# Optimization experiments

Hardware: AMD Instinct MI355X
Metric: run time of the kernel (lower is better)

The kernel has to match this reference:

```python
import jax, jax.numpy as jnp
import numpy as np

B, N, J, P = 64, 2048, 32, 64   # instances, ops per instance, jobs, ops per job (N = J*P)
D, H = 128, 128                 # out_size_ope, hidden_size_ope
NEG_SLOPE = 0.2


def _kaiming(key, fan_in, fan_out):
    return jax.random.normal(key, (fan_in, fan_out), jnp.float32) * np.sqrt(2.0 / fan_in)


def _mlp(x, W1, b1, W2, b2):
    # nn.Sequential(Linear, ELU, Linear)
    return jax.nn.elu(x @ W1 + b1) @ W2 + b2


def setup_inputs() -> dict:
    key = jax.random.key(0)
    ks = jax.random.split(key, 4)
    features = jax.random.normal(ks[0], (B, N, D), jnp.float32)
    job_starts = jnp.arange(J, dtype=jnp.int32) * P                      # first op of each job block
    offsets = jax.random.randint(ks[1], (B, J), 0, P)                    # current position within block
    ope_step_batch = job_starts[None, :] + offsets                       # [B, J], step_j in [start_j, end_j]
    end_ope_biases_batch = jnp.broadcast_to(job_starts + (P - 1), (B, J))
    opes_appertain_batch = jnp.broadcast_to(jnp.repeat(jnp.arange(J, dtype=jnp.int32), P)[None, :], (B, N))
    batch_idxes = jnp.arange(B, dtype=jnp.int32)
    inp = {
        'features': features,
        'discount_r': jnp.float32(0.9),
        'ope_step_batch': ope_step_batch,
        'end_ope_biases_batch': end_ope_biases_batch,
        'opes_appertain_batch': opes_appertain_batch,
        'batch_idxes': batch_idxes,
    }
    for i, nm in enumerate(['fw', 'zj', 'pr']):
        k1, k2 = jax.random.split(jax.random.fold_in(ks[2], i))
        inp[nm + '_W1'] = _kaiming(k1, D, H)
        inp[nm + '_b1'] = jnp.zeros((H,), jnp.float32)
        inp[nm + '_W2'] = _kaiming(k2, H, D)
        inp[nm + '_b2'] = jnp.zeros((D,), jnp.float32)
    return inp


def reference(features, discount_r,
              fw_W1, fw_b1, fw_W2, fw_b2,
              zj_W1, zj_b1, zj_W2, zj_b2,
              pr_W1, pr_b1, pr_W2, pr_b2,
              ope_step_batch, end_ope_biases_batch, opes_appertain_batch, batch_idxes):
    # opes_appertain_batch is accepted but unused, exactly like the torch forward.
    f32 = features.dtype
    steps = ope_step_batch[batch_idxes]        # [B, J]
    ends = end_ope_biases_batch[batch_idxes]   # [B, J]
    i = jnp.arange(N)

    # --- per-job descending update loop, vectorized ---
    # op i is updated iff step_j < i <= end_j for its job j; descending order in the
    # original means feat[i-1] is still the ORIGINAL value, so updates are independent.
    memb = (i[None, None, :] > steps[:, :, None]) & (i[None, None, :] <= ends[:, :, None])  # [B,J,N]
    updated = jnp.any(memb, axis=1)                                                         # [B,N]
    step_of = jnp.sum(jnp.where(memb, steps[:, :, None], 0), axis=1)                        # [B,N]
    rpow = discount_r ** (i[None, :] - step_of).astype(f32)                                 # r^(i - step)
    feat_prev = jnp.concatenate([jnp.zeros_like(features[:, :1]), features[:, :-1]], axis=1)
    # aggregate(MEAN): agg_f_w(feat_pre) + agg_f_w(feat_sub * r)
    cand = _mlp(features, fw_W1, fw_b1, fw_W2, fw_b2) + \
           _mlp(feat_prev * rpow[..., None], fw_W1, fw_b1, fw_W2, fw_b2)
    feat1 = jnp.where(updated[..., None], cand, features)

    # --- collect feat at each valid job's current step (step positions are never updated) ---
    collected = jax.vmap(lambda f, s: f[s])(features, steps)   # [B, J, D]
    valid = steps <= ends                                      # [B, J]
    n = jnp.sum(valid, axis=1).astype(f32)                     # [B]
    S = jnp.sum(jnp.where(valid[..., None], collected, 0.0), axis=1)  # [B, D]
    # aggregate_dif: new[j] = agg_z_j((old[j] + r * sum_{k!=j} old[k]) / n)
    mixed = (collected + discount_r * (S[:, None, :] - collected)) / n[:, None, None]
    z = _mlp(mixed, zj_W1, zj_b1, zj_W2, zj_b2)                # [B, J, D]

    # faithful replication of feat_opt[b][save_index[k]] = features_all[k]
    # (writes at op positions equal to JOB indices 0..J-1, for valid jobs)
    head = jnp.where(valid[..., None], z, feat1[:, :J, :])
    feat2 = feat1.at[:, :J, :].set(head)

    out = jax.nn.leaky_relu(_mlp(feat2, pr_W1, pr_b1, pr_W2, pr_b2), NEG_SLOPE)
    return out
```

## Files before the change

### kernel.cpp

```cpp
#include <hip/hip_runtime.h>

#define B_ 64
#define N_ 2048
#define J_ 32
#define D_ 128
#define NEG_SLOPE_ 0.2f

typedef __attribute__((ext_vector_type(4))) float f32x4;
typedef __attribute__((ext_vector_type(8))) __bf16 bf16x8;
typedef __attribute__((ext_vector_type(4))) __bf16 bf16x4;

#define ACT_NONE 0
#define ACT_ELU 1
#define ACT_LEAKY 2

template<int ACT>
__device__ __forceinline__ float apply_act(float v) {
    if constexpr (ACT == ACT_ELU)        return v > 0.f ? v : __expf(v) - 1.f;
    else if constexpr (ACT == ACT_LEAKY) return v >= 0.f ? v : NEG_SLOPE_ * v;
    else return v;
}

__device__ __forceinline__ bf16x8 frag_ld(const __bf16* src, int row, int kc) {
    return *(const bf16x8*)&src[row * D_ + ((kc ^ (row & 7)) << 3)];
}

__device__ __forceinline__ void load_wregs2(const __bf16* __restrict__ wmat,
                                            int wst, int ln, int lq, bf16x8 wr_[4][2]) {
#pragma unroll
    for (int ks = 0; ks < 4; ++ks)
#pragma unroll
        for (int mt = 0; mt < 2; ++mt)
            wr_[ks][mt] = frag_ld(wmat, wst * 32 + mt * 16 + ln, ks * 4 + lq);
}

__device__ __forceinline__ void st_row(__bf16* dst, int row, int ch,
                                       float4 f0, float4 f1, float s) {
    bf16x8 u;
    u[0] = (__bf16)(f0.x * s); u[1] = (__bf16)(f0.y * s);
    u[2] = (__bf16)(f0.z * s); u[3] = (__bf16)(f0.w * s);
    u[4] = (__bf16)(f1.x * s); u[5] = (__bf16)(f1.y * s);
    u[6] = (__bf16)(f1.z * s); u[7] = (__bf16)(f1.w * s);
    *(bf16x8*)&dst[row * D_ + ((ch ^ (row & 7)) << 3)] = u;
}

template<bool INIT>
__device__ __forceinline__ void gemmS32(const __bf16* xb, const bf16x8 wr_[4][2],
                                        int ln, int lq, f32x4 acc[2][2]) {
    if constexpr (INIT) {
        const f32x4 z = {0.f, 0.f, 0.f, 0.f};
        acc[0][0] = z; acc[0][1] = z; acc[1][0] = z; acc[1][1] = z;
    }
#pragma unroll
    for (int ks = 0; ks < 4; ++ks) {
        const int kc = ks * 4 + lq;
        const bf16x8 b0 = frag_ld(xb, ln, kc);
        const bf16x8 b1 = frag_ld(xb, 16 + ln, kc);
#pragma unroll
        for (int mt = 0; mt < 2; ++mt) {
            acc[mt][0] = __builtin_amdgcn_mfma_f32_16x16x32_bf16(wr_[ks][mt], b0, acc[mt][0], 0, 0, 0);
            acc[mt][1] = __builtin_amdgcn_mfma_f32_16x16x32_bf16(wr_[ks][mt], b1, acc[mt][1], 0, 0, 0);
        }
    }
}

template<int ACT>
__device__ __forceinline__ void epiS32_lds(const f32x4 acc[2][2], __bf16* dst, int rowoff,
                                           const float* __restrict__ bias,
                                           int wst, int ln, int lq) {
#pragma unroll
    for (int mt = 0; mt < 2; ++mt) {
        const int cb = wst * 32 + mt * 16 + lq * 4;
        const f32x4 bv = *(const f32x4*)&bias[cb];
#pragma unroll
        for (int nt = 0; nt < 2; ++nt) {
            const int jr = rowoff + nt * 16 + ln;
            bf16x4 o;
#pragma unroll
            for (int r = 0; r < 4; ++r)
                o[r] = (__bf16)apply_act<ACT>(acc[mt][nt][r] + bv[r]);
            *(bf16x4*)&dst[jr * D_ + (((cb >> 3) ^ (jr & 7)) << 3) + (cb & 7)] = o;
        }
    }
}

__global__ __launch_bounds__(256) void k_prep(
    const float* __restrict__ w0, const float* __restrict__ w1,
    const float* __restrict__ w2, const float* __restrict__ w3,
    const float* __restrict__ w4, const float* __restrict__ w5,
    __bf16* __restrict__ wdst,
    const float* __restrict__ F, const int* __restrict__ STEP,
    const int* __restrict__ ENDB, const int* __restrict__ BIDX,
    float* __restrict__ Sbuf, int* __restrict__ nvalid) {
    const int t = threadIdx.x;
    if (blockIdx.x < 6) {
        const float* src;
        switch (blockIdx.x) {
            case 0: src = w0; break; case 1: src = w1; break; case 2: src = w2; break;
            case 3: src = w3; break; case 4: src = w4; break; default: src = w5; break;
        }
        __bf16* d = wdst + (size_t)blockIdx.x * D_ * D_;
        for (int id = t; id < D_ * 16; id += 256) {
            const int n = id >> 4, ch = id & 15;
            bf16x8 u;
#pragma unroll
            for (int j = 0; j < 8; ++j) u[j] = (__bf16)src[(ch * 8 + j) * D_ + n];
            *(bf16x8*)&d[n * D_ + ((ch ^ (n & 7)) << 3)] = u;
        }
        return;
    }
    const int b = blockIdx.x - 6;
    __shared__ int steps_s[J_];
    __shared__ int valid_s[J_];
    __shared__ int nv;
    const int bi = BIDX[b];
    if (t == 0) nv = 0;
    __syncthreads();
    if (t < J_) {
        const int s = STEP[bi * J_ + t];
        const int e = ENDB[bi * J_ + t];
        steps_s[t] = s;
        const int v = (s <= e) ? 1 : 0;
        valid_s[t] = v;
        if (v) atomicAdd(&nv, 1);
    }
    __syncthreads();
    if (t < D_) {
        float acc = 0.f;
        for (int j = 0; j < J_; ++j)
            if (valid_s[j]) acc += F[((size_t)b * N_ + steps_s[j]) * D_ + t];
        Sbuf[b * D_ + t] = acc;
    }
    if (t == 0) nvalid[b] = nv;
}

__global__ __launch_bounds__(256, 4) void k_fused(
    const float* __restrict__ F, const float* __restrict__ rp_,
    const __bf16* __restrict__ wsW,
    const float* __restrict__ fb1, const float* __restrict__ fb2,
    const float* __restrict__ zb1, const float* __restrict__ zb2,
    const float* __restrict__ pb1, const float* __restrict__ pb2,
    const int* __restrict__ STEP, const int* __restrict__ ENDB,
    const int* __restrict__ BIDX, const float* __restrict__ Sbuf,
    const int* __restrict__ nvalid, float* __restrict__ out) {
    __shared__ __bf16 xs[64 * D_];
    __shared__ __bf16 hs[32 * D_];

    const int t = threadIdx.x;
    const int lane = t & 63, wst = t >> 6;
    const int ln = lane & 15, lq = lane >> 4;
    const int bid = blockIdx.x;
    const int b = bid >> 6, ti = bid & 63;
    const int r0 = ti * 32;
    const int bi = BIDX[b];
    const int jb = ti >> 1;
    const int s_j = STEP[bi * J_ + jb];
    const int e_j = ENDB[bi * J_ + jb];
    const float r = *rp_;
    const float l2r = __log2f(r);
    const int lo = (s_j + 1 > r0) ? s_j + 1 : r0;
    const int hi = (e_j < r0 + 31) ? e_j : r0 + 31;
    const bool has_upd = lo <= hi;
    const bool head_tile = (ti == 0);

    const float* Fb = F + (size_t)b * N_ * D_;
    const int rr_ = t >> 4;
    const int ch_ = t & 15;
    const int rA = r0 + rr_, rB = rA + 16;
    const float* qA = Fb + (size_t)rA * D_ + ch_ * 8;
    const float* qB = Fb + (size_t)rB * D_ + ch_ * 8;
    const float4 xa0 = *(const float4*)qA, xa1 = *(const float4*)(qA + 4);
    const float4 xb0 = *(const float4*)qB, xb1 = *(const float4*)(qB + 4);
    float4 ya0, ya1, yb0, yb1;
    float scA = 0.f, scB = 0.f;
    if (has_upd) {
        const bool uA = (rA > s_j) && (rA <= e_j);
        const bool uB = (rB > s_j) && (rB <= e_j);
        scA = uA ? exp2f((float)(rA - s_j) * l2r) : 0.f;
        scB = uB ? exp2f((float)(rB - s_j) * l2r) : 0.f;
        const float* uqA = Fb + (size_t)(uA ? rA - 1 : rA) * D_ + ch_ * 8;
        const float* uqB = Fb + (size_t)(uB ? rB - 1 : rB) * D_ + ch_ * 8;
        ya0 = *(const float4*)uqA; ya1 = *(const float4*)(uqA + 4);
        yb0 = *(const float4*)uqB; yb1 = *(const float4*)(uqB + 4);
    }
    bf16x8 wA[4][2];
    load_wregs2(has_upd ? wsW : wsW + 2 * 16384, wst, ln, lq, wA);

    st_row(xs, rr_, ch_, xa0, xa1, 1.f);
    st_row(xs, rr_ + 16, ch_, xb0, xb1, 1.f);
    if (has_upd) {
        st_row(xs, rr_ + 32, ch_, ya0, ya1, scA);
        st_row(xs, rr_ + 48, ch_, yb0, yb1, scB);
    }
    __syncthreads();

    if (has_upd) {
        f32x4 acc[2][2];
        gemmS32<true>(xs, wA, ln, lq, acc);
        bf16x8 wB[4][2];
        load_wregs2(wsW + 16384, wst, ln, lq, wB);
        epiS32_lds<ACT_ELU>(acc, hs, 0, fb1, wst, ln, lq);
        __syncthreads();
        f32x4 a2[2][2];
        gemmS32<true>(hs, wB, ln, lq, a2);
        __syncthreads();
        gemmS32<true>(xs + 32 * D_, wA, ln, lq, acc);
        epiS32_lds<ACT_ELU>(acc, hs, 0, fb1, wst, ln, lq);
        __syncthreads();
        gemmS32<false>(hs, wB, ln, lq, a2);
#pragma unroll
        for (int nt = 0; nt < 2; ++nt) {
            const int row = nt * 16 + ln;
            const int i = r0 + row;
            if (!((i > s_j) && (i <= e_j))) continue;
#pragma unroll
            for (int mt = 0; mt < 2; ++mt) {
                const int cb = wst * 32 + mt * 16 + lq * 4;
                const f32x4 bv = *(const f32x4*)&fb2[cb];
                bf16x4 o;
#pragma unroll
                for (int rr2 = 0; rr2 < 4; ++rr2)
                    o[rr2] = (__bf16)(a2[mt][nt][rr2] + 2.f * bv[rr2]);
                *(bf16x4*)&xs[row * D_ + (((cb >> 3) ^ (row & 7)) << 3) + (cb & 7)] = o;
            }
        }
    }

    if (head_tile) {
        __syncthreads();
        const float n_ = (float)nvalid[b];
        const float inv = (n_ > 0.f) ? 1.f / n_ : 0.f;
#pragma unroll
        for (int it = 0; it < 2; ++it) {
            const int id = t + it * 256;
            const int row = id >> 4, ch = id & 15;
            const int sr = STEP[bi * J_ + row];
            const float* cr = Fb + (size_t)sr * D_ + ch * 8;
            const float4 c0 = *(const float4*)cr, c1 = *(const float4*)(cr + 4);
            const float4 s0 = *(const float4*)(Sbuf + b * D_ + ch * 8);
            const float4 s1 = *(const float4*)(Sbuf + b * D_ + ch * 8 + 4);
            bf16x8 u;
            u[0] = (__bf16)((c0.x + r * (s0.x - c0.x)) * inv);
            u[1] = (__bf16)((c0.y + r * (s0.y - c0.y)) * inv);
            u[2] = (__bf16)((c0.z + r * (s0.z - c0.z)) * inv);
            u[3] = (__bf16)((c0.w + r * (s0.w - c0.w)) * inv);
            u[4] = (__bf16)((c1.x + r * (s1.x - c1.x)) * inv);
            u[5] = (__bf16)((c1.y + r * (s1.y - c1.y)) * inv);
            u[6] = (__bf16)((c1.z + r * (s1.z - c1.z)) * inv);
            u[7] = (__bf16)((c1.w + r * (s1.w - c1.w)) * inv);
            *(bf16x8*)&hs[row * D_ + ((ch ^ (row & 7)) << 3)] = u;
        }
        __syncthreads();
        {
            bf16x8 wza[4][2];
            load_wregs2(wsW + 4 * 16384, wst, ln, lq, wza);
            f32x4 az[2][2];
            gemmS32<true>(hs, wza, ln, lq, az);
            epiS32_lds<ACT_ELU>(az, xs, 32, zb1, wst, ln, lq);
        }
        __syncthreads();
        {
            bf16x8 wzb[4][2];
            load_wregs2(wsW + 5 * 16384, wst, ln, lq, wzb);
            f32x4 az[2][2];
            gemmS32<true>(xs + 32 * D_, wzb, ln, lq, az);
#pragma unroll
            for (int nt = 0; nt < 2; ++nt) {
                const int row = nt * 16 + ln;
                const int sr = STEP[bi * J_ + row];
                const int er = ENDB[bi * J_ + row];
                if (sr > er) continue;
#pragma unroll
                for (int mt = 0; mt < 2; ++mt) {
                    const int cb = wst * 32 + mt * 16 + lq * 4;
                    const f32x4 bv = *(const f32x4*)&zb2[cb];
                    bf16x4 o;
#pragma unroll
                    for (int rr2 = 0; rr2 < 4; ++rr2)
                        o[rr2] = (__bf16)(az[mt][nt][rr2] + bv[rr2]);
                    *(bf16x4*)&xs[row * D_ + (((cb >> 3) ^ (row & 7)) << 3) + (cb & 7)] = o;
                }
            }
        }
    }

    if (has_upd || head_tile)
        load_wregs2(wsW + 2 * 16384, wst, ln, lq, wA);
    __syncthreads();

    f32x4 ap[2][2];
    gemmS32<true>(xs, wA, ln, lq, ap);
    bf16x8 wB2[4][2];
    load_wregs2(wsW + 3 * 16384, wst, ln, lq, wB2);
    epiS32_lds<ACT_ELU>(ap, hs, 0, pb1, wst, ln, lq);
    __syncthreads();

    gemmS32<true>(hs, wB2, ln, lq, ap);
    float* outb = out + ((size_t)b * N_ + r0) * D_;
#pragma unroll
    for (int mt = 0; mt < 2; ++mt) {
        const int cb = wst * 32 + mt * 16 + lq * 4;
        const f32x4 bv = *(const f32x4*)&pb2[cb];
#pragma unroll
        for (int nt = 0; nt < 2; ++nt) {
            const int jr = nt * 16 + ln;
            f32x4 o;
#pragma unroll
            for (int rr2 = 0; rr2 < 4; ++rr2)
                o[rr2] = apply_act<ACT_LEAKY>(ap[mt][nt][rr2] + bv[rr2]);
            *(f32x4*)&outb[(size_t)jr * D_ + cb] = o;
        }
    }
}

extern "C" void kernel_launch(void* const* d_in, const int* in_sizes, int n_in,
                              void* d_out, int out_size, void* d_ws, size_t ws_size,
                              hipStream_t stream) {
    const float* F    = (const float*)d_in[0];
    const float* rp   = (const float*)d_in[1];
    const int*  STEP  = (const int*)d_in[2];
    const int*  ENDB  = (const int*)d_in[3];
    const int*  BIDX  = (const int*)d_in[5];
    const float* fwW1 = (const float*)d_in[6];
    const float* fwb1 = (const float*)d_in[7];
    const float* fwW2 = (const float*)d_in[8];
    const float* fwb2 = (const float*)d_in[9];
    const float* zjW1 = (const float*)d_in[10];
    const float* zjb1 = (const float*)d_in[11];
    const float* zjW2 = (const float*)d_in[12];
    const float* zjb2 = (const float*)d_in[13];
    const float* prW1 = (const float*)d_in[14];
    const float* prb1 = (const float*)d_in[15];
    const float* prW2 = (const float*)d_in[16];
    const float* prb2 = (const float*)d_in[17];
    float* out = (float*)d_out;

    char* ws = (char*)d_ws;
    __bf16* wsW = (__bf16*)ws;
    float* Sbuf = (float*)(ws + 393216);
    int* nvalid = (int*)(ws + 425984);

    hipLaunchKernelGGL(k_prep, dim3(70), dim3(256), 0, stream,
                       fwW1, fwW2, prW1, prW2, zjW1, zjW2, wsW,
                       F, STEP, ENDB, BIDX, Sbuf, nvalid);
    hipLaunchKernelGGL(k_fused, dim3(B_ * 64), dim3(256), 0, stream,
                       F, rp, wsW, fwb1, fwb2, zjb1, zjb2, prb1, prb2,
                       STEP, ENDB, BIDX, Sbuf, nvalid, out);
}
```

Baseline: 71.61 us.

## Split fused MLP tile across 8 waves with 16-column slices per wave

Doubles the block to 512 threads so each of 8 waves owns a 16-column output slice instead of 32, halving per-wave weight registers and accumulators. The two first-layer fw GEMMs now run as a single 64-row GEMM, with both hidden halves kept in a larger hs buffer, which removes a couple of barriers. The z-MLP intermediate moves into hs, and the pre-projection barrier is skipped for tiles that need no update. The aim is more waves in flight and lower register pressure to hide latency, at the cost of twice the LDS per block and more redundant B-fragment LDS reads across waves.

```diff
diff --git a/kernel.cpp b/kernel.cpp
--- a/kernel.cpp
+++ b/kernel.cpp
@@ -25,13 +25,11 @@
     return *(const bf16x8*)&src[row * D_ + ((kc ^ (row & 7)) << 3)];
 }
 
-__device__ __forceinline__ void load_wregs2(const __bf16* __restrict__ wmat,
-                                            int wst, int ln, int lq, bf16x8 wr_[4][2]) {
+__device__ __forceinline__ void load_wregs1(const __bf16* __restrict__ wmat,
+                                            int wst, int ln, int lq, bf16x8 wr_[4]) {
 #pragma unroll
     for (int ks = 0; ks < 4; ++ks)
-#pragma unroll
-        for (int mt = 0; mt < 2; ++mt)
-            wr_[ks][mt] = frag_ld(wmat, wst * 32 + mt * 16 + ln, ks * 4 + lq);
+        wr_[ks] = frag_ld(wmat, wst * 16 + ln, ks * 4 + lq);
 }
 
 __device__ __forceinline__ void st_row(__bf16* dst, int row, int ch,
@@ -44,43 +42,70 @@
     *(bf16x8*)&dst[row * D_ + ((ch ^ (row & 7)) << 3)] = u;
 }
 
+__device__ __forceinline__ void gemmS64(const __bf16* xb, const bf16x8 wr_[4],
+                                        int ln, int lq, f32x4 acc[4]) {
+    const f32x4 z = {0.f, 0.f, 0.f, 0.f};
+#pragma unroll
+    for (int nt = 0; nt < 4; ++nt) acc[nt] = z;
+#pragma unroll
+    for (int ks = 0; ks < 4; ++ks) {
+        const int kc = ks * 4 + lq;
+#pragma unroll
+        for (int nt = 0; nt < 4; ++nt) {
+            const bf16x8 b = frag_ld(xb, nt * 16 + ln, kc);
+            acc[nt] = __builtin_amdgcn_mfma_f32_16x16x32_bf16(wr_[ks], b, acc[nt], 0, 0, 0);
+        }
+    }
+}
+
 template<bool INIT>
-__device__ __forceinline__ void gemmS32(const __bf16* xb, const bf16x8 wr_[4][2],
-                                        int ln, int lq, f32x4 acc[2][2]) {
+__device__ __forceinline__ void gemmS32(const __bf16* xb, const bf16x8 wr_[4],
+                                        int ln, int lq, f32x4 acc[2]) {
     if constexpr (INIT) {
         const f32x4 z = {0.f, 0.f, 0.f, 0.f};
-        acc[0][0] = z; acc[0][1] = z; acc[1][0] = z; acc[1][1] = z;
+        acc[0] = z; acc[1] = z;
     }
 #pragma unroll
     for (int ks = 0; ks < 4; ++ks) {
         const int kc = ks * 4 + lq;
         const bf16x8 b0 = frag_ld(xb, ln, kc);
         const bf16x8 b1 = frag_ld(xb, 16 + ln, kc);
-#pragma unroll
-        for (int mt = 0; mt < 2; ++mt) {
-            acc[mt][0] = __builtin_amdgcn_mfma_f32_16x16x32_bf16(wr_[ks][mt], b0, acc[mt][0], 0, 0, 0);
-            acc[mt][1] = __builtin_amdgcn_mfma_f32_16x16x32_bf16(wr_[ks][mt], b1, acc[mt][1], 0, 0, 0);
-        }
+        acc[0] = __builtin_amdgcn_mfma_f32_16x16x32_bf16(wr_[ks], b0, acc[0], 0, 0, 0);
+        acc[1] = __builtin_amdgcn_mfma_f32_16x16x32_bf16(wr_[ks], b1, acc[1], 0, 0, 0);
     }
 }
 
 template<int ACT>
-__device__ __forceinline__ void epiS32_lds(const f32x4 acc[2][2], __bf16* dst, int rowoff,
+__device__ __forceinline__ void epiS64_lds(const f32x4 acc[4], __bf16* dst,
                                            const float* __restrict__ bias,
                                            int wst, int ln, int lq) {
-#pragma unroll
-    for (int mt = 0; mt < 2; ++mt) {
-        const int cb = wst * 32 + mt * 16 + lq * 4;
-        const f32x4 bv = *(const f32x4*)&bias[cb];
-#pragma unroll
-        for (int nt = 0; nt < 2; ++nt) {
-            const int jr = rowoff + nt * 16 + ln;
-            bf16x4 o;
-#pragma unroll
-            for (int r = 0; r < 4; ++r)
-                o[r] = (__bf16)apply_act<ACT>(acc[mt][nt][r] + bv[r]);
-            *(bf16x4*)&dst[jr * D_ + (((cb >> 3) ^ (jr & 7)) << 3) + (cb & 7)] = o;
-        }
+    const int cb = wst * 16 + lq * 4;
+    const f32x4 bv = *(const f32x4*)&bias[cb];
+#pragma unroll
+    for (int nt = 0; nt < 4; ++nt) {
+        const int jr = nt * 16 + ln;
+        bf16x4 o;
+#pragma unroll
+        for (int r = 0; r < 4; ++r)
+            o[r] = (__bf16)apply_act<ACT>(acc[nt][r] + bv[r]);
+        *(bf16x4*)&dst[jr * D_ + (((cb >> 3) ^ (jr & 7)) << 3) + (cb & 7)] = o;
+    }
+}
+
+template<int ACT>
+__device__ __forceinline__ void epiS32_lds(const f32x4 acc[2], __bf16* dst, int rowoff,
+                                           const float* __restrict__ bias,
+                                           int wst, int ln, int lq) {
+    const int cb = wst * 16 + lq * 4;
+    const f32x4 bv = *(const f32x4*)&bias[cb];
+#pragma unroll
+    for (int nt = 0; nt < 2; ++nt) {
+        const int jr = rowoff + nt * 16 + ln;
+        bf16x4 o;
+#pragma unroll
+        for (int r = 0; r < 4; ++r)
+            o[r] = (__bf16)apply_act<ACT>(acc[nt][r] + bv[r]);
+        *(bf16x4*)&dst[jr * D_ + (((cb >> 3) ^ (jr & 7)) << 3) + (cb & 7)] = o;
     }
 }
 
@@ -134,7 +159,7 @@
     if (t == 0) nvalid[b] = nv;
 }
 
-__global__ __launch_bounds__(256, 4) void k_fused(
+__global__ __launch_bounds__(512, 8) void k_fused(
     const float* __restrict__ F, const float* __restrict__ rp_,
     const __bf16* __restrict__ wsW,
     const float* __restrict__ fb1, const float* __restrict__ fb2,
@@ -144,7 +169,7 @@
     const int* __restrict__ BIDX, const float* __restrict__ Sbuf,
     const int* __restrict__ nvalid, float* __restrict__ out) {
     __shared__ __bf16 xs[64 * D_];
-    __shared__ __bf16 hs[32 * D_];
+    __shared__ __bf16 hs[64 * D_];
 
     const int t = threadIdx.x;
     const int lane = t & 63, wst = t >> 6;
@@ -166,63 +191,46 @@
     const float* Fb = F + (size_t)b * N_ * D_;
     const int rr_ = t >> 4;
     const int ch_ = t & 15;
-    const int rA = r0 + rr_, rB = rA + 16;
+    const int rA = r0 + rr_;
     const float* qA = Fb + (size_t)rA * D_ + ch_ * 8;
-    const float* qB = Fb + (size_t)rB * D_ + ch_ * 8;
     const float4 xa0 = *(const float4*)qA, xa1 = *(const float4*)(qA + 4);
-    const float4 xb0 = *(const float4*)qB, xb1 = *(const float4*)(qB + 4);
-    float4 ya0, ya1, yb0, yb1;
-    float scA = 0.f, scB = 0.f;
+    float4 ya0, ya1;
+    float scA = 0.f;
     if (has_upd) {
         const bool uA = (rA > s_j) && (rA <= e_j);
-        const bool uB = (rB > s_j) && (rB <= e_j);
         scA = uA ? exp2f((float)(rA - s_j) * l2r) : 0.f;
-        scB = uB ? exp2f((float)(rB - s_j) * l2r) : 0.f;
         const float* uqA = Fb + (size_t)(uA ? rA - 1 : rA) * D_ + ch_ * 8;
-        const float* uqB = Fb + (size_t)(uB ? rB - 1 : rB) * D_ + ch_ * 8;
         ya0 = *(const float4*)uqA; ya1 = *(const float4*)(uqA + 4);
-        yb0 = *(const float4*)uqB; yb1 = *(const float4*)(uqB + 4);
-    }
-    bf16x8 wA[4][2];
-    load_wregs2(has_upd ? wsW : wsW + 2 * 16384, wst, ln, lq, wA);
+    }
+    bf16x8 wA[4];
+    load_wregs1(has_upd ? wsW : wsW + 2 * 16384, wst, ln, lq, wA);
 
     st_row(xs, rr_, ch_, xa0, xa1, 1.f);
-    st_row(xs, rr_ + 16, ch_, xb0, xb1, 1.f);
+    if (has_upd) st_row(xs, rr_ + 32, ch_, ya0, ya1, scA);
+    __syncthreads();
+
     if (has_upd) {
-        st_row(xs, rr_ + 32, ch_, ya0, ya1, scA);
-        st_row(xs, rr_ + 48, ch_, yb0, yb1, scB);
-    }
-    __syncthreads();
-
-    if (has_upd) {
-        f32x4 acc[2][2];
-        gemmS32<true>(xs, wA, ln, lq, acc);
-        bf16x8 wB[4][2];
-        load_wregs2(wsW + 16384, wst, ln, lq, wB);
-        epiS32_lds<ACT_ELU>(acc, hs, 0, fb1, wst, ln, lq);
-        __syncthreads();
-        f32x4 a2[2][2];
+        f32x4 acc[4];
+        gemmS64(xs, wA, ln, lq, acc);
+        bf16x8 wB[4];
+        load_wregs1(wsW + 16384, wst, ln, lq, wB);
+        epiS64_lds<ACT_ELU>(acc, hs, fb1, wst, ln, lq);
+        __syncthreads();
+        f32x4 a2[2];
         gemmS32<true>(hs, wB, ln, lq, a2);
-        __syncthreads();
-        gemmS32<true>(xs + 32 * D_, wA, ln, lq, acc);
-        epiS32_lds<ACT_ELU>(acc, hs, 0, fb1, wst, ln, lq);
-        __syncthreads();
-        gemmS32<false>(hs, wB, ln, lq, a2);
+        gemmS32<false>(hs + 32 * D_, wB, ln, lq, a2);
+        const int cb = wst * 16 + lq * 4;
+        const f32x4 bv = *(const f32x4*)&fb2[cb];
 #pragma unroll
         for (int nt = 0; nt < 2; ++nt) {
             const int row = nt * 16 + ln;
             const int i = r0 + row;
             if (!((i > s_j) && (i <= e_j))) continue;
-#pragma unroll
-            for (int mt = 0; mt < 2; ++mt) {
-                const int cb = wst * 32 + mt * 16 + lq * 4;
-                const f32x4 bv = *(const f32x4*)&fb2[cb];
-                bf16x4 o;
-#pragma unroll
-                for (int rr2 = 0; rr2 < 4; ++rr2)
-                    o[rr2] = (__bf16)(a2[mt][nt][rr2] + 2.f * bv[rr2]);
-                *(bf16x4*)&xs[row * D_ + (((cb >> 3) ^ (row & 7)) << 3) + (cb & 7)] = o;
-            }
+            bf16x4 o;
+#pragma unroll
+            for (int rr2 = 0; rr2 < 4; ++rr2)
+                o[rr2] = (__bf16)(a2[nt][rr2] + 2.f * bv[rr2]);
+            *(bf16x4*)&xs[row * D_ + (((cb >> 3) ^ (row & 7)) << 3) + (cb & 7)] = o;
         }
     }
 
@@ -230,10 +238,8 @@
         __syncthreads();
         const float n_ = (float)nvalid[b];
         const float inv = (n_ > 0.f) ? 1.f / n_ : 0.f;
-#pragma unroll
-        for (int it = 0; it < 2; ++it) {
-            const int id = t + it * 256;
-            const int row = id >> 4, ch = id & 15;
+        {
+            const int row = t >> 4, ch = t & 15;
             const int sr = STEP[bi * J_ + row];
             const float* cr = Fb + (size_t)sr * D_ + ch * 8;
             const float4 c0 = *(const float4*)cr, c1 = *(const float4*)(cr + 4);
@@ -252,64 +258,59 @@
         }
         __syncthreads();
         {
-            bf16x8 wza[4][2];
-            load_wregs2(wsW + 4 * 16384, wst, ln, lq, wza);
-            f32x4 az[2][2];
+            bf16x8 wza[4];
+            load_wregs1(wsW + 4 * 16384, wst, ln, lq, wza);
+            f32x4 az[2];
             gemmS32<true>(hs, wza, ln, lq, az);
-            epiS32_lds<ACT_ELU>(az, xs, 32, zb1, wst, ln, lq);
+            epiS32_lds<ACT_ELU>(az, hs, 32, zb1, wst, ln, lq);
         }
         __syncthreads();
         {
-            bf16x8 wzb[4][2];
-            load_wregs2(wsW + 5 * 16384, wst, ln, lq, wzb);
-            f32x4 az[2][2];
-            gemmS32<true>(xs + 32 * D_, wzb, ln, lq, az);
+            bf16x8 wzb[4];
+            load_wregs1(wsW + 5 * 16384, wst, ln, lq, wzb);
+            f32x4 az[2];
+            gemmS32<true>(hs + 32 * D_, wzb, ln, lq, az);
+            const int cb = wst * 16 + lq * 4;
+            const f32x4 bv = *(const f32x4*)&zb2[cb];
 #pragma unroll
             for (int nt = 0; nt < 2; ++nt) {
                 const int row = nt * 16 + ln;
                 const int sr = STEP[bi * J_ + row];
                 const int er = ENDB[bi * J_ + row];
                 if (sr > er) continue;
-#pragma unroll
-                for (int mt = 0; mt < 2; ++mt) {
-                    const int cb = wst * 32 + mt * 16 + lq * 4;
-                    const f32x4 bv = *(const f32x4*)&zb2[cb];
-                    bf16x4 o;
-#pragma unroll
-                    for (int rr2 = 0; rr2 < 4; ++rr2)
-                        o[rr2] = (__bf16)(az[mt][nt][rr2] + bv[rr2]);
-                    *(bf16x4*)&xs[row * D_ + (((cb >> 3) ^ (row & 7)) << 3) + (cb & 7)] = o;
-                }
+                bf16x4 o;
+#pragma unroll
+                for (int rr2 = 0; rr2 < 4; ++rr2)
+                    o[rr2] = (__bf16)(az[nt][rr2] + bv[rr2]);
+                *(bf16x4*)&xs[row * D_ + (((cb >> 3) ^ (row & 7)) << 3) + (cb & 7)] = o;
             }
         }
     }
 
-    if (has_upd || head_tile)
-        load_wregs2(wsW + 2 * 16384, wst, ln, lq, wA);
-    __syncthreads();
-
-    f32x4 ap[2][2];
+    if (has_upd || head_tile) {
+        load_wregs1(wsW + 2 * 16384, wst, ln, lq, wA);
+        __syncthreads();
+    }
+
+    f32x4 ap[2];
     gemmS32<true>(xs, wA, ln, lq, ap);
-    bf16x8 wB2[4][2];
-    load_wregs2(wsW + 3 * 16384, wst, ln, lq, wB2);
+    bf16x8 wB2[4];
+    load_wregs1(wsW + 3 * 16384, wst, ln, lq, wB2);
     epiS32_lds<ACT_ELU>(ap, hs, 0, pb1, wst, ln, lq);
     __syncthreads();
 
     gemmS32<true>(hs, wB2, ln, lq, ap);
     float* outb = out + ((size_t)b * N_ + r0) * D_;
-#pragma unroll
-    for (int mt = 0; mt < 2; ++mt) {
-        const int cb = wst * 32 + mt * 16 + lq * 4;
-        const f32x4 bv = *(const f32x4*)&pb2[cb];
-#pragma unroll
-        for (int nt = 0; nt < 2; ++nt) {
-            const int jr = nt * 16 + ln;
-            f32x4 o;
-#pragma unroll
-            for (int rr2 = 0; rr2 < 4; ++rr2)
-                o[rr2] = apply_act<ACT_LEAKY>(ap[mt][nt][rr2] + bv[rr2]);
-            *(f32x4*)&outb[(size_t)jr * D_ + cb] = o;
-        }
+    const int cb = wst * 16 + lq * 4;
+    const f32x4 bv = *(const f32x4*)&pb2[cb];
+#pragma unroll
+    for (int nt = 0; nt < 2; ++nt) {
+        const int jr = nt * 16 + ln;
+        f32x4 o;
+#pragma unroll
+        for (int rr2 = 0; rr2 < 4; ++rr2)
+            o[rr2] = apply_act<ACT_LEAKY>(ap[nt][rr2] + bv[rr2]);
+        *(f32x4*)&outb[(size_t)jr * D_ + cb] = o;
     }
 }
 
@@ -343,7 +344,7 @@
     hipLaunchKernelGGL(k_prep, dim3(70), dim3(256), 0, stream,
                        fwW1, fwW2, prW1, prW2, zjW1, zjW2, wsW,
                        F, STEP, ENDB, BIDX, Sbuf, nvalid);
-    hipLaunchKernelGGL(k_fused, dim3(B_ * 64), dim3(256), 0, stream,
+    hipLaunchKernelGGL(k_fused, dim3(B_ * 64), dim3(512), 0, stream,
                        F, rp, wsW, fwb1, fwb2, zjb1, zjb2, prb1, prb2,
                        STEP, ENDB, BIDX, Sbuf, nvalid, out);
 }
```

Result: slower. 77.04 us (+7.6%).
